# Kernel tuning notes

Hardware: AMD Instinct MI355X
Metric: run time of the kernel (lower is better)

The kernel has to match this reference:

```python
import jax, jax.numpy as jnp
import numpy as np
from jax import lax

B, N, C = 32, 512, 512   # N must be 8*8*8 (Convpass reshape)
H, DH = 8, 64            # heads, head_dim
ADIM = 8                 # adapter dim
MLP = 4096
EPS = 1e-5
SCALE = DH ** -0.5


def _ln(x, g, b):
    m = jnp.mean(x, axis=-1, keepdims=True)
    v = jnp.mean((x - m) ** 2, axis=-1, keepdims=True)
    return (x - m) * lax.rsqrt(v + EPS) * g + b


def _qgelu(x):
    return x * jax.nn.sigmoid(1.702 * x)


def _convpass(x, dw, db, cw, cb, uw, ub):
    # x: [B,N,C] -> down [B,N,ADIM]
    d = _qgelu(jnp.einsum('bnc,ca->bna', x, dw) + db)
    p = d.reshape(B, 8, 8, 8, ADIM).transpose(0, 4, 1, 2, 3)  # NCDHW
    p = lax.conv_general_dilated(
        p, cw, window_strides=(1, 1, 1), padding='SAME',
        dimension_numbers=('NCDHW', 'OIDHW', 'NCDHW')) + cb[None, :, None, None, None]
    p = p.transpose(0, 2, 3, 4, 1).reshape(B, N, ADIM)
    return jnp.einsum('bna,ac->bnc', _qgelu(p), uw) + ub


def _attn(x, qkv_w, proj_w, proj_b):
    qkv = jnp.einsum('bnc,ck->bnk', x, qkv_w)            # [B,N,3C]
    qkv = qkv.reshape(B, N, 3, H, DH)
    q, k, v = (qkv[:, :, i].transpose(0, 2, 1, 3) for i in range(3))  # [B,H,N,DH]
    a = jax.nn.softmax(jnp.einsum('bhnd,bhmd->bhnm', q, k) * SCALE, axis=-1)
    o = jnp.einsum('bhnm,bhmd->bhnd', a, v).transpose(0, 2, 1, 3).reshape(B, N, C)
    return jnp.einsum('bnc,ck->bnk', o, proj_w) + proj_b


def setup_inputs() -> dict:
    key = jax.random.key(0)
    ks = jax.random.split(key, 24)
    r = lambda i, shape, s=0.02: jax.random.normal(ks[i], shape, jnp.float32) * s
    inp = {
        'x': jax.random.normal(ks[0], (B, N, C), jnp.float32),
        'pos': jax.random.normal(ks[1], (B, N, C), jnp.float32),
        'ln1_g': jnp.ones((C,), jnp.float32), 'ln1_b': jnp.zeros((C,), jnp.float32),
        'qkv_w': r(2, (C, 3 * C)),
        'proj_w': r(3, (C, C)), 'proj_b': jnp.zeros((C,), jnp.float32),
        'cp1_down_w': r(4, (C, ADIM)), 'cp1_down_b': jnp.zeros((ADIM,), jnp.float32),
        'cp1_conv_w': r(5, (ADIM, ADIM, 3, 3, 3), 0.1), 'cp1_conv_b': jnp.zeros((ADIM,), jnp.float32),
        'cp1_up_w': r(6, (ADIM, C)), 'cp1_up_b': jnp.zeros((C,), jnp.float32),
        'ln2_g': jnp.ones((C,), jnp.float32), 'ln2_b': jnp.zeros((C,), jnp.float32),
        'ff_w1': r(7, (C, MLP)), 'ff_b1': jnp.zeros((MLP,), jnp.float32),
        'ff_w2': r(8, (MLP, C)), 'ff_b2': jnp.zeros((C,), jnp.float32),
        'cp2_down_w': r(9, (C, ADIM)), 'cp2_down_b': jnp.zeros((ADIM,), jnp.float32),
        'cp2_conv_w': r(10, (ADIM, ADIM, 3, 3, 3), 0.1), 'cp2_conv_b': jnp.zeros((ADIM,), jnp.float32),
        'cp2_up_w': r(11, (ADIM, C)), 'cp2_up_b': jnp.zeros((C,), jnp.float32),
    }
    return inp


def reference(x, pos, ln1_g, ln1_b, qkv_w, proj_w, proj_b,
              cp1_down_w, cp1_down_b, cp1_conv_w, cp1_conv_b, cp1_up_w, cp1_up_b,
              ln2_g, ln2_b, ff_w1, ff_b1, ff_w2, ff_b2,
              cp2_down_w, cp2_down_b, cp2_conv_w, cp2_conv_b, cp2_up_w, cp2_up_b):
    x = x + pos
    # attention stage: Residual(PreNormDrop(LN, SelfAttn, Convpass)), dropout=identity (eval)
    h = _ln(x, ln1_g, ln1_b)
    x = x + _attn(h, qkv_w, proj_w, proj_b) + _convpass(h, cp1_down_w, cp1_down_b, cp1_conv_w, cp1_conv_b, cp1_up_w, cp1_up_b)
    # FFN stage: Residual(PreNorm(LN, FFN, Convpass))
    h = _ln(x, ln2_g, ln2_b)
    ffn = jnp.einsum('bnm,mc->bnc', jax.nn.gelu(jnp.einsum('bnc,cm->bnm', h, ff_w1) + ff_b1, approximate=False), ff_w2) + ff_b2
    x = x + ffn + _convpass(h, cp2_down_w, cp2_down_b, cp2_conv_w, cp2_conv_b, cp2_up_w, cp2_up_b)
    return x
```

## Files before the change

kernel.cpp:

```cpp
#include <hip/hip_runtime.h>
#include <math.h>

typedef __bf16 bf16_t;
typedef __bf16 bf16x8 __attribute__((ext_vector_type(8)));
typedef float f32x4 __attribute__((ext_vector_type(4)));

constexpr int kB   = 32;
constexpr int kN   = 512;
constexpr int kC   = 512;
constexpr int kH   = 8;
constexpr int kAD  = 8;
constexpr int kMLP = 4096;
constexpr int kBN  = kB * kN;
constexpr float kEPS   = 1e-5f;
constexpr float kSCALE = 0.125f;

__device__ __forceinline__ float qgelu_f(float x) {
    return x / (1.f + __expf(-1.702f * x));
}
__device__ __forceinline__ float gelu_f(float x) {
    float u = 1.5957691216f * x * (1.f + 0.044715f * x * x);
    float e = __expf(u);
    float th = 1.f - 2.f / (e + 1.f);
    return 0.5f * x * (1.f + th);
}

__device__ __forceinline__ void gld_lds16(const void* g, void* l) {
    typedef const __attribute__((address_space(1))) unsigned int* gp_t;
    typedef __attribute__((address_space(3))) unsigned int* lp_t;
    __builtin_amdgcn_global_load_lds((gp_t)(unsigned long long)g,
                                     (lp_t)(unsigned)(unsigned long long)l,
                                     16, 0, 0);
}

__global__ __launch_bounds__(256) void k_addln(
    const float* __restrict__ x, const float* __restrict__ pos,
    const float* __restrict__ g, const float* __restrict__ be,
    float* __restrict__ xout, bf16_t* __restrict__ hout,
    const float* __restrict__ cpv, const float* __restrict__ uwp,
    const float* __restrict__ ubp)
{
    int row = blockIdx.x, tid = threadIdx.x;
    size_t base = (size_t)row * kC;
    __shared__ float s8[8];
    if (cpv) {
        if (tid < 8) s8[tid] = cpv[(size_t)row * 8 + tid];
        __syncthreads();
    }
    float v0 = x[base + tid], v1 = x[base + tid + 256];
    if (pos) { v0 += pos[base + tid]; v1 += pos[base + tid + 256]; }
    if (cpv) {
        float u0 = ubp[tid], u1 = ubp[tid + 256];
        #pragma unroll
        for (int a = 0; a < 8; a++) {
            u0 += s8[a] * uwp[a * kC + tid];
            u1 += s8[a] * uwp[a * kC + tid + 256];
        }
        v0 += u0; v1 += u1;
    }
    if (xout) { xout[base + tid] = v0; xout[base + tid + 256] = v1; }
    float s = v0 + v1, q = v0 * v0 + v1 * v1;
    #pragma unroll
    for (int o = 32; o > 0; o >>= 1) {
        s += __shfl_down(s, o);
        q += __shfl_down(q, o);
    }
    __shared__ float ss[4], sq[4], mrs[2];
    int wv = tid >> 6, ln = tid & 63;
    if (!ln) { ss[wv] = s; sq[wv] = q; }
    __syncthreads();
    if (!tid) {
        float ts = ss[0] + ss[1] + ss[2] + ss[3];
        float tq = sq[0] + sq[1] + sq[2] + sq[3];
        float m = ts * (1.f / kC);
        float var = tq * (1.f / kC) - m * m;
        mrs[0] = m; mrs[1] = rsqrtf(var + kEPS);
    }
    __syncthreads();
    float m = mrs[0], r = mrs[1];
    hout[base + tid]       = (bf16_t)((v0 - m) * r * g[tid] + be[tid]);
    hout[base + tid + 256] = (bf16_t)((v1 - m) * r * g[tid + 256] + be[tid + 256]);
}

__global__ __launch_bounds__(256) void k_transpose_all(
    const float* __restrict__ qkvw, const float* __restrict__ projw,
    const float* __restrict__ fw1,  const float* __restrict__ fw2,
    bf16_t* __restrict__ qkvT, bf16_t* __restrict__ projT,
    bf16_t* __restrict__ fw1T, bf16_t* __restrict__ fw2T)
{
    int id = blockIdx.x;
    const float* w; bf16_t* wt; int K, N, bx, by;
    if (id < 768)       { w = qkvw; wt = qkvT; K = 512;  N = 1536; bx = id % 48;  by = id / 48; }
    else if (id < 1024) { id -= 768;  w = projw; wt = projT; K = 512;  N = 512;  bx = id % 16;  by = id / 16; }
    else if (id < 3072) { id -= 1024; w = fw1;   wt = fw1T;  K = 512;  N = 4096; bx = id % 128; by = id / 128; }
    else                { id -= 3072; w = fw2;   wt = fw2T;  K = 4096; N = 512;  bx = id % 16;  by = id / 16; }
    __shared__ float t[32][33];
    int n0 = bx * 32, k0 = by * 32;
    int tx = threadIdx.x & 31, ty = threadIdx.x >> 5;
    #pragma unroll
    for (int j = 0; j < 32; j += 8)
        t[ty + j][tx] = w[(size_t)(k0 + ty + j) * N + n0 + tx];
    __syncthreads();
    #pragma unroll
    for (int j = 0; j < 32; j += 8)
        wt[(size_t)(n0 + ty + j) * K + k0 + tx] = (bf16_t)t[tx][ty + j];
}

template <int ACT, bool HASB, bool HASR, int OMODE, int K, int LDA, int LDB, int NC>
__global__ __launch_bounds__(256) void k_gemm(
    const bf16_t* __restrict__ A, const bf16_t* __restrict__ Bt,
    const float* __restrict__ bias, const float* __restrict__ res,
    void* __restrict__ outv)
{
    __shared__ bf16_t As[2][128 * 32];
    __shared__ bf16_t Bs[2][128 * 32];
    int tid = threadIdx.x;
    int col0 = blockIdx.x * 128, row0 = blockIdx.y * 128;
    int w = tid >> 6, l = tid & 63;
    int rw0 = (w & 1) * 64, cw0 = (w >> 1) * 64;
    int lr = tid >> 2;
    int lc = (((tid & 3) ^ ((tid >> 3) & 3)) * 8);

    f32x4 acc[4][4];
    #pragma unroll
    for (int i = 0; i < 4; i++)
        #pragma unroll
        for (int j = 0; j < 4; j++)
            acc[i][j] = (f32x4){0.f, 0.f, 0.f, 0.f};

    const bf16_t* Ag  = A  + (size_t)(row0 + lr) * LDA + lc;
    const bf16_t* Ag2 = A  + (size_t)(row0 + 64 + lr) * LDA + lc;
    const bf16_t* Bg  = Bt + (size_t)(col0 + lr) * LDB + lc;
    const bf16_t* Bg2 = Bt + (size_t)(col0 + 64 + lr) * LDB + lc;

    int am = rw0 + (l & 15);
    int bn = cw0 + (l & 15);
    int kq = (l >> 4) * 8;
    int kqA = kq ^ (((am >> 1) & 3) << 3);
    int kqB = kq ^ (((bn >> 1) & 3) << 3);

    for (int k0 = 0; k0 < K; k0 += 64) {
        gld_lds16(Ag + k0, &As[0][tid * 8]);
        gld_lds16(Ag2 + k0, &As[0][2048 + tid * 8]);
        gld_lds16(Bg + k0, &Bs[0][tid * 8]);
        gld_lds16(Bg2 + k0, &Bs[0][2048 + tid * 8]);
        gld_lds16(Ag + k0 + 32, &As[1][tid * 8]);
        gld_lds16(Ag2 + k0 + 32, &As[1][2048 + tid * 8]);
        gld_lds16(Bg + k0 + 32, &Bs[1][tid * 8]);
        gld_lds16(Bg2 + k0 + 32, &Bs[1][2048 + tid * 8]);
        __syncthreads();
        #pragma unroll
        for (int ks = 0; ks < 2; ks++) {
            bf16x8 af[4], bfr[4];
            #pragma unroll
            for (int mt = 0; mt < 4; mt++)
                af[mt] = *(const bf16x8*)&As[ks][(am + mt * 16) * 32 + kqA];
            #pragma unroll
            for (int nt = 0; nt < 4; nt++)
                bfr[nt] = *(const bf16x8*)&Bs[ks][(bn + nt * 16) * 32 + kqB];
            #pragma unroll
            for (int mt = 0; mt < 4; mt++)
                #pragma unroll
                for (int nt = 0; nt < 4; nt++)
                    acc[mt][nt] = __builtin_amdgcn_mfma_f32_16x16x32_bf16(
                        af[mt], bfr[nt], acc[mt][nt], 0, 0, 0);
        }
        __syncthreads();
    }

    #pragma unroll
    for (int mt = 0; mt < 4; mt++) {
        int rowb = row0 + rw0 + mt * 16 + (l >> 4) * 4;
        #pragma unroll
        for (int nt = 0; nt < 4; nt++) {
            int col = col0 + cw0 + nt * 16 + (l & 15);
            float bv = HASB ? bias[col] : 0.f;
            #pragma unroll
            for (int p = 0; p < 4; p++) {
                float v = acc[mt][nt][p] + bv;
                if (ACT == 1) v = qgelu_f(v);
                if (ACT == 2) v = gelu_f(v);
                int r = rowb + p;
                if (OMODE == 0) {
                    if (HASR) v += res[(size_t)r * NC + col];
                    ((float*)outv)[(size_t)r * NC + col] = v;
                } else if (OMODE == 1) {
                    ((bf16_t*)outv)[(size_t)r * NC + col] = (bf16_t)v;
                } else {
                    int bb = r >> 9, n = r & 511;
                    int which = col >> 9, hd = (col >> 6) & 7, d = col & 63;
                    ((bf16_t*)outv)[(((size_t)(bb * 8 + hd) * 3 + which) << 15)
                                    + n * 64 + d] = (bf16_t)v;
                }
            }
        }
    }
}

__global__ __launch_bounds__(256) void k_attn(
    const bf16_t* __restrict__ qkvb, bf16_t* __restrict__ obuf)
{
    __shared__ bf16_t Ks[64 * 72];
    __shared__ bf16_t Vt[64 * 72];
    __shared__ bf16_t Ps[4][32 * 72];
    int bid = blockIdx.x;
    int qb = bid & 3, h = (bid >> 2) & 7, b = bid >> 5;
    int t = threadIdx.x, w = t >> 6, l = t & 63;
    const bf16_t* qp = qkvb + (((size_t)(b * 8 + h) * 3) << 15);
    const bf16_t* kp = qp + (1 << 15);
    const bf16_t* vp = qp + (2 << 15);
    int q0 = qb * 128 + w * 32;
    int l15 = l & 15, lq = (l >> 4) * 8;

    bf16x8 aq[2][2];
    #pragma unroll
    for (int mt = 0; mt < 2; mt++)
        #pragma unroll
        for (int kh = 0; kh < 2; kh++)
            aq[mt][kh] = *(const bf16x8*)(qp + (size_t)(q0 + mt * 16 + l15) * 64
                                          + kh * 32 + lq);

    f32x4 o[2][4];
    float m_run[2][4], l_run[2][4];
    #pragma unroll
    for (int mt = 0; mt < 2; mt++) {
        #pragma unroll
        for (int dt = 0; dt < 4; dt++) o[mt][dt] = (f32x4){0.f, 0.f, 0.f, 0.f};
        #pragma unroll
        for (int p = 0; p < 4; p++) { m_run[mt][p] = -1e30f; l_run[mt][p] = 0.f; }
    }

    int sr = t >> 2, scc = (t & 3) * 16;
    for (int kt = 0; kt < 8; kt++) {
        if (kt) __syncthreads();
        {
            const bf16_t* ks = kp + (size_t)(kt * 64 + sr) * 64 + scc;
            *(uint4*)&Ks[sr * 72 + scc]     = *(const uint4*)ks;
            *(uint4*)&Ks[sr * 72 + scc + 8] = *(const uint4*)(ks + 8);
            const bf16_t* vs = vp + (size_t)(kt * 64 + sr) * 64 + scc;
            bf16x8 v0 = *(const bf16x8*)vs;
            bf16x8 v1 = *(const bf16x8*)(vs + 8);
            #pragma unroll
            for (int e = 0; e < 8; e++) {
                Vt[(scc + e) * 72 + sr]     = v0[e];
                Vt[(scc + 8 + e) * 72 + sr] = v1[e];
            }
        }
        __syncthreads();
        #pragma unroll
        for (int mt = 0; mt < 2; mt++) {
            f32x4 sc[4];
            #pragma unroll
            for (int nt = 0; nt < 4; nt++) sc[nt] = (f32x4){0.f, 0.f, 0.f, 0.f};
            #pragma unroll
            for (int nt = 0; nt < 4; nt++)
                #pragma unroll
                for (int kh = 0; kh < 2; kh++) {
                    bf16x8 bk = *(const bf16x8*)&Ks[(nt * 16 + l15) * 72
                                                    + kh * 32 + lq];
                    sc[nt] = __builtin_amdgcn_mfma_f32_16x16x32_bf16(
                        aq[mt][kh], bk, sc[nt], 0, 0, 0);
                }
            #pragma unroll
            for (int nt = 0; nt < 4; nt++)
                #pragma unroll
                for (int p = 0; p < 4; p++) sc[nt][p] *= kSCALE;

            float mx[4], alpha[4], rs[4];
            #pragma unroll
            for (int p = 0; p < 4; p++) {
                float m4 = fmaxf(fmaxf(sc[0][p], sc[1][p]),
                                 fmaxf(sc[2][p], sc[3][p]));
                #pragma unroll
                for (int off = 1; off < 16; off <<= 1)
                    m4 = fmaxf(m4, __shfl_xor(m4, off));
                float mn = fmaxf(m_run[mt][p], m4);
                alpha[p] = __expf(m_run[mt][p] - mn);
                m_run[mt][p] = mn;
                mx[p] = mn;
                rs[p] = 0.f;
            }
            int prow = mt * 16 + (l >> 4) * 4;
            #pragma unroll
            for (int nt = 0; nt < 4; nt++)
                #pragma unroll
                for (int p = 0; p < 4; p++) {
                    float pv = __expf(sc[nt][p] - mx[p]);
                    rs[p] += pv;
                    Ps[w][(prow + p) * 72 + nt * 16 + l15] = (bf16_t)pv;
                }
            #pragma unroll
            for (int p = 0; p < 4; p++) {
                float r = rs[p];
                #pragma unroll
                for (int off = 1; off < 16; off <<= 1)
                    r += __shfl_xor(r, off);
                l_run[mt][p] = l_run[mt][p] * alpha[p] + r;
                #pragma unroll
                for (int dt = 0; dt < 4; dt++) o[mt][dt][p] *= alpha[p];
            }
            bf16x8 ap[2];
            #pragma unroll
            for (int kh = 0; kh < 2; kh++)
                ap[kh] = *(const bf16x8*)&Ps[w][(mt * 16 + l15) * 72
                                                + kh * 32 + lq];
            #pragma unroll
            for (int dt = 0; dt < 4; dt++)
                #pragma unroll
                for (int kh = 0; kh < 2; kh++) {
                    bf16x8 bv = *(const bf16x8*)&Vt[(dt * 16 + l15) * 72
                                                    + kh * 32 + lq];
                    o[mt][dt] = __builtin_amdgcn_mfma_f32_16x16x32_bf16(
                        ap[kh], bv, o[mt][dt], 0, 0, 0);
                }
        }
    }
    #pragma unroll
    for (int mt = 0; mt < 2; mt++)
        #pragma unroll
        for (int dt = 0; dt < 4; dt++)
            #pragma unroll
            for (int p = 0; p < 4; p++) {
                int q = q0 + mt * 16 + (l >> 4) * 4 + p;
                int col = h * 64 + dt * 16 + l15;
                float v = o[mt][dt][p] / l_run[mt][p];
                obuf[((size_t)b * 512 + q) * 512 + col] = (bf16_t)v;
            }
}

__global__ __launch_bounds__(256) void k_down(
    const bf16_t* __restrict__ h, const float* __restrict__ dw,
    const float* __restrict__ db, float* __restrict__ outp)
{
    __shared__ float sdw[kC * kAD];
    int t = threadIdx.x;
    for (int i = t; i < kC * kAD; i += 256) sdw[i] = dw[i];
    __syncthreads();
    int gt = blockIdx.x * 256 + t;
    int row = gt >> 3, a = gt & 7;
    const bf16x8* hr = (const bf16x8*)(h + (size_t)row * kC);
    float acc = 0.f;
    for (int k8 = 0; k8 < kC / 8; k8++) {
        bf16x8 hv = hr[k8];
        #pragma unroll
        for (int e = 0; e < 8; e++)
            acc += (float)hv[e] * sdw[(k8 * 8 + e) * kAD + a];
    }
    outp[gt] = qgelu_f(acc + db[a]);
}

__global__ __launch_bounds__(512) void k_conv(
    const float* __restrict__ inp, const float* __restrict__ cw,
    const float* __restrict__ cb, float* __restrict__ outp)
{
    __shared__ float si[512 * 9];
    __shared__ float sw[8 * 8 * 27];
    int b = blockIdx.x, t = threadIdx.x;
    for (int i = t; i < 512 * 8; i += 512) {
        int n = i >> 3, a = i & 7;
        si[n * 9 + a] = inp[(size_t)b * 4096 + i];
    }
    for (int i = t; i < 1728; i += 512) sw[i] = cw[i];
    __syncthreads();
    int z = t >> 6, y = (t >> 3) & 7, xx = t & 7;
    float acc[8];
    #pragma unroll
    for (int ao = 0; ao < 8; ao++) acc[ao] = cb[ao];
    for (int dz = -1; dz <= 1; dz++) {
        int zz = z + dz; if ((unsigned)zz > 7u) continue;
        for (int dy = -1; dy <= 1; dy++) {
            int yy = y + dy; if ((unsigned)yy > 7u) continue;
            for (int dx = -1; dx <= 1; dx++) {
                int xn = xx + dx; if ((unsigned)xn > 7u) continue;
                int nn = zz * 64 + yy * 8 + xn;
                int wo = ((dz + 1) * 3 + (dy + 1)) * 3 + (dx + 1);
                #pragma unroll
                for (int ai = 0; ai < 8; ai++) {
                    float iv = si[nn * 9 + ai];
                    #pragma unroll
                    for (int ao = 0; ao < 8; ao++)
                        acc[ao] += iv * sw[(ao * 8 + ai) * 27 + wo];
                }
            }
        }
    }
    #pragma unroll
    for (int ao = 0; ao < 8; ao++)
        outp[(size_t)b * 4096 + t * 8 + ao] = qgelu_f(acc[ao]);
}

__global__ __launch_bounds__(256) void k_up(
    const float* __restrict__ pa, const float* __restrict__ uw,
    const float* __restrict__ ub, float* __restrict__ xbuf)
{
    __shared__ float s[8];
    int row = blockIdx.x, t = threadIdx.x;
    if (t < 8) s[t] = pa[(size_t)row * kAD + t];
    __syncthreads();
    #pragma unroll
    for (int rep = 0; rep < 2; rep++) {
        int c = t + rep * 256;
        float acc = ub[c];
        #pragma unroll
        for (int a = 0; a < 8; a++) acc += s[a] * uw[a * kC + c];
        xbuf[(size_t)row * kC + c] += acc;
    }
}

extern "C" void kernel_launch(void* const* d_in, const int* in_sizes, int n_in,
                              void* d_out, int out_size, void* d_ws, size_t ws_size,
                              hipStream_t stream)
{
    const float* x     = (const float*)d_in[0];
    const float* pos   = (const float*)d_in[1];
    const float* ln1g  = (const float*)d_in[2];
    const float* ln1b  = (const float*)d_in[3];
    const float* qkvw  = (const float*)d_in[4];
    const float* projw = (const float*)d_in[5];
    const float* projb = (const float*)d_in[6];
    const float* dw1   = (const float*)d_in[7];
    const float* db1   = (const float*)d_in[8];
    const float* cw1   = (const float*)d_in[9];
    const float* cb1   = (const float*)d_in[10];
    const float* uw1   = (const float*)d_in[11];
    const float* ub1   = (const float*)d_in[12];
    const float* ln2g  = (const float*)d_in[13];
    const float* ln2b  = (const float*)d_in[14];
    const float* fw1   = (const float*)d_in[15];
    const float* fb1   = (const float*)d_in[16];
    const float* fw2   = (const float*)d_in[17];
    const float* fb2   = (const float*)d_in[18];
    const float* dw2   = (const float*)d_in[19];
    const float* db2   = (const float*)d_in[20];
    const float* cw2   = (const float*)d_in[21];
    const float* cb2   = (const float*)d_in[22];
    const float* uw2   = (const float*)d_in[23];
    const float* ub2   = (const float*)d_in[24];
    float* out = (float*)d_out;

    char* wsb = (char*)d_ws;
    float*  xbuf = (float*)wsb;
    bf16_t* hb   = (bf16_t*)(wsb + 33554432);
    bf16_t* obuf = (bf16_t*)(wsb + 50331648);
    bf16_t* qkvb = (bf16_t*)(wsb + 67108864);
    bf16_t* midb = (bf16_t*)(wsb + 50331648);
    bf16_t* qkvT = (bf16_t*)(wsb + 117440512);
    bf16_t* projT= (bf16_t*)(wsb + 119013376);
    bf16_t* fw1T = (bf16_t*)(wsb + 119537664);
    bf16_t* fw2T = (bf16_t*)(wsb + 123731968);
    float*  cpa  = (float*)(wsb + 127926272);
    float*  cpb  = (float*)(wsb + 128450560);

    k_transpose_all<<<5120, 256, 0, stream>>>(
        qkvw, projw, fw1, fw2, qkvT, projT, fw1T, fw2T);

    k_addln<<<kBN, 256, 0, stream>>>(x, pos, ln1g, ln1b, xbuf, hb,
                                     nullptr, nullptr, nullptr);

    k_gemm<0, false, false, 2, 512, 512, 512, 1536>
        <<<dim3(12, 128), 256, 0, stream>>>(hb, qkvT, nullptr, nullptr, qkvb);
    k_attn<<<kB * kH * 4, 256, 0, stream>>>(qkvb, obuf);
    k_gemm<0, true, true, 0, 512, 512, 512, 512>
        <<<dim3(4, 128), 256, 0, stream>>>(obuf, projT, projb, xbuf, xbuf);

    k_down<<<kBN * kAD / 256, 256, 0, stream>>>(hb, dw1, db1, cpa);
    k_conv<<<kB, 512, 0, stream>>>(cpa, cw1, cb1, cpb);

    k_addln<<<kBN, 256, 0, stream>>>(xbuf, nullptr, ln2g, ln2b, xbuf, hb,
                                     cpb, uw1, ub1);

    k_down<<<kBN * kAD / 256, 256, 0, stream>>>(hb, dw2, db2, cpa);
    k_conv<<<kB, 512, 0, stream>>>(cpa, cw2, cb2, cpb);
    k_up<<<kBN, 256, 0, stream>>>(cpb, uw2, ub2, xbuf);

    k_gemm<2, true, false, 1, 512, 512, 512, 2048>
        <<<dim3(16, 128), 256, 0, stream>>>(hb, fw1T, fb1, nullptr, midb);
    k_gemm<0, false, true, 0, 2048, 2048, 4096, 512>
        <<<dim3(4, 128), 256, 0, stream>>>(midb, fw2T, nullptr, xbuf, xbuf);
    k_gemm<2, true, false, 1, 512, 512, 512, 2048>
        <<<dim3(16, 128), 256, 0, stream>>>(hb, fw1T + (size_t)2048 * 512,
                                            fb1 + 2048, nullptr, midb);
    k_gemm<0, true, true, 0, 2048, 2048, 4096, 512>
        <<<dim3(4, 128), 256, 0, stream>>>(midb, fw2T + 2048, fb2, xbuf, out);
}
```

Measured before the change: 639.9 us.

## Store V transposed from QKV GEMM and compute transposed attention from registers

The QKV GEMM epilogue now writes V transposed (d-major) using packed 4-wide stores. The attention kernel then loads K and V^T fragments straight from global memory into registers, so the shared-memory staging, the scalar transpose and the block barriers are gone. It also computes S^T so each lane owns one query column, which cuts the softmax reductions to two shuffles, and it pre-scales Q by the softmax scale. The P tile goes through a small per-warp LDS buffer, and the output is written with packed stores. The cost is that K and V are re-read from global or L2 by every warp instead of being shared through LDS, and rounding Q after scaling changes precision slightly.

```diff
diff --git a/kernel.cpp b/kernel.cpp
--- a/kernel.cpp
+++ b/kernel.cpp
@@ -3,6 +3,7 @@
 
 typedef __bf16 bf16_t;
 typedef __bf16 bf16x8 __attribute__((ext_vector_type(8)));
+typedef __bf16 bf16x4 __attribute__((ext_vector_type(4)));
 typedef float f32x4 __attribute__((ext_vector_type(4)));
 
 constexpr int kB   = 32;
@@ -23,6 +24,12 @@
     float e = __expf(u);
     float th = 1.f - 2.f / (e + 1.f);
     return 0.5f * x * (1.f + th);
+}
+
+__device__ __forceinline__ unsigned pk2(float a, float b) {
+    union { bf16_t h[2]; unsigned u; } z;
+    z.h[0] = (bf16_t)a; z.h[1] = (bf16_t)b;
+    return z.u;
 }
 
 __device__ __forceinline__ void gld_lds16(const void* g, void* l) {
@@ -175,22 +182,34 @@
         for (int nt = 0; nt < 4; nt++) {
             int col = col0 + cw0 + nt * 16 + (l & 15);
             float bv = HASB ? bias[col] : 0.f;
-            #pragma unroll
-            for (int p = 0; p < 4; p++) {
-                float v = acc[mt][nt][p] + bv;
-                if (ACT == 1) v = qgelu_f(v);
-                if (ACT == 2) v = gelu_f(v);
-                int r = rowb + p;
-                if (OMODE == 0) {
-                    if (HASR) v += res[(size_t)r * NC + col];
-                    ((float*)outv)[(size_t)r * NC + col] = v;
-                } else if (OMODE == 1) {
-                    ((bf16_t*)outv)[(size_t)r * NC + col] = (bf16_t)v;
+            if (OMODE == 2) {
+                int which = col >> 9, hd = (col >> 6) & 7, d = col & 63;
+                size_t hb = ((size_t)((rowb >> 9) * 8 + hd) * 3 + which) << 15;
+                int n0 = rowb & 511;
+                if (which == 2) {
+                    bf16x4 pk;
+                    #pragma unroll
+                    for (int p = 0; p < 4; p++) pk[p] = (bf16_t)acc[mt][nt][p];
+                    *(bf16x4*)((bf16_t*)outv + hb + (size_t)d * 512 + n0) = pk;
                 } else {
-                    int bb = r >> 9, n = r & 511;
-                    int which = col >> 9, hd = (col >> 6) & 7, d = col & 63;
-                    ((bf16_t*)outv)[(((size_t)(bb * 8 + hd) * 3 + which) << 15)
-                                    + n * 64 + d] = (bf16_t)v;
+                    #pragma unroll
+                    for (int p = 0; p < 4; p++)
+                        ((bf16_t*)outv)[hb + (size_t)(n0 + p) * 64 + d] =
+                            (bf16_t)acc[mt][nt][p];
+                }
+            } else {
+                #pragma unroll
+                for (int p = 0; p < 4; p++) {
+                    float v = acc[mt][nt][p] + bv;
+                    if (ACT == 1) v = qgelu_f(v);
+                    if (ACT == 2) v = gelu_f(v);
+                    int r = rowb + p;
+                    if (OMODE == 0) {
+                        if (HASR) v += res[(size_t)r * NC + col];
+                        ((float*)outv)[(size_t)r * NC + col] = v;
+                    } else {
+                        ((bf16_t*)outv)[(size_t)r * NC + col] = (bf16_t)v;
+                    }
                 }
             }
         }
@@ -200,53 +219,53 @@
 __global__ __launch_bounds__(256) void k_attn(
     const bf16_t* __restrict__ qkvb, bf16_t* __restrict__ obuf)
 {
-    __shared__ bf16_t Ks[64 * 72];
-    __shared__ bf16_t Vt[64 * 72];
-    __shared__ bf16_t Ps[4][32 * 72];
+    __shared__ __align__(16) unsigned Ps[4][16 * 36];
     int bid = blockIdx.x;
     int qb = bid & 3, h = (bid >> 2) & 7, b = bid >> 5;
     int t = threadIdx.x, w = t >> 6, l = t & 63;
-    const bf16_t* qp = qkvb + (((size_t)(b * 8 + h) * 3) << 15);
-    const bf16_t* kp = qp + (1 << 15);
-    const bf16_t* vp = qp + (2 << 15);
+    const bf16_t* qp  = qkvb + (((size_t)(b * 8 + h) * 3) << 15);
+    const bf16_t* kp  = qp + (1 << 15);
+    const bf16_t* vtp = qp + (2 << 15);
     int q0 = qb * 128 + w * 32;
-    int l15 = l & 15, lq = (l >> 4) * 8;
+    int l15 = l & 15, g = l >> 4, lq = g * 8;
+    unsigned* psw = &Ps[w][0];
 
     bf16x8 aq[2][2];
     #pragma unroll
     for (int mt = 0; mt < 2; mt++)
         #pragma unroll
-        for (int kh = 0; kh < 2; kh++)
-            aq[mt][kh] = *(const bf16x8*)(qp + (size_t)(q0 + mt * 16 + l15) * 64
-                                          + kh * 32 + lq);
+        for (int kh = 0; kh < 2; kh++) {
+            bf16x8 qv = *(const bf16x8*)(qp + (size_t)(q0 + mt * 16 + l15) * 64
+                                         + kh * 32 + lq);
+            #pragma unroll
+            for (int e = 0; e < 8; e++) qv[e] = (bf16_t)((float)qv[e] * kSCALE);
+            aq[mt][kh] = qv;
+        }
 
     f32x4 o[2][4];
-    float m_run[2][4], l_run[2][4];
+    float m_run[2], l_run[2];
     #pragma unroll
     for (int mt = 0; mt < 2; mt++) {
+        m_run[mt] = -1e30f; l_run[mt] = 0.f;
         #pragma unroll
         for (int dt = 0; dt < 4; dt++) o[mt][dt] = (f32x4){0.f, 0.f, 0.f, 0.f};
-        #pragma unroll
-        for (int p = 0; p < 4; p++) { m_run[mt][p] = -1e30f; l_run[mt][p] = 0.f; }
-    }
-
-    int sr = t >> 2, scc = (t & 3) * 16;
+    }
+
     for (int kt = 0; kt < 8; kt++) {
-        if (kt) __syncthreads();
-        {
-            const bf16_t* ks = kp + (size_t)(kt * 64 + sr) * 64 + scc;
-            *(uint4*)&Ks[sr * 72 + scc]     = *(const uint4*)ks;
-            *(uint4*)&Ks[sr * 72 + scc + 8] = *(const uint4*)(ks + 8);
-            const bf16_t* vs = vp + (size_t)(kt * 64 + sr) * 64 + scc;
-            bf16x8 v0 = *(const bf16x8*)vs;
-            bf16x8 v1 = *(const bf16x8*)(vs + 8);
-            #pragma unroll
-            for (int e = 0; e < 8; e++) {
-                Vt[(scc + e) * 72 + sr]     = v0[e];
-                Vt[(scc + 8 + e) * 72 + sr] = v1[e];
-            }
-        }
-        __syncthreads();
+        bf16x8 kf[4][2], vf[4][2];
+        #pragma unroll
+        for (int nt = 0; nt < 4; nt++)
+            #pragma unroll
+            for (int kh = 0; kh < 2; kh++)
+                kf[nt][kh] = *(const bf16x8*)(kp
+                    + (size_t)(kt * 64 + nt * 16 + l15) * 64 + kh * 32 + lq);
+        #pragma unroll
+        for (int dt = 0; dt < 4; dt++)
+            #pragma unroll
+            for (int kh = 0; kh < 2; kh++)
+                vf[dt][kh] = *(const bf16x8*)(vtp
+                    + (size_t)(dt * 16 + l15) * 512 + kt * 64 + kh * 32 + lq);
+
         #pragma unroll
         for (int mt = 0; mt < 2; mt++) {
             f32x4 sc[4];
@@ -255,77 +274,66 @@
             #pragma unroll
             for (int nt = 0; nt < 4; nt++)
                 #pragma unroll
-                for (int kh = 0; kh < 2; kh++) {
-                    bf16x8 bk = *(const bf16x8*)&Ks[(nt * 16 + l15) * 72
-                                                    + kh * 32 + lq];
+                for (int kh = 0; kh < 2; kh++)
                     sc[nt] = __builtin_amdgcn_mfma_f32_16x16x32_bf16(
-                        aq[mt][kh], bk, sc[nt], 0, 0, 0);
+                        kf[nt][kh], aq[mt][kh], sc[nt], 0, 0, 0);
+            float mx = sc[0][0];
+            #pragma unroll
+            for (int nt = 0; nt < 4; nt++)
+                #pragma unroll
+                for (int p = 0; p < 4; p++) mx = fmaxf(mx, sc[nt][p]);
+            mx = fmaxf(mx, __shfl_xor(mx, 16));
+            mx = fmaxf(mx, __shfl_xor(mx, 32));
+            float mn = fmaxf(m_run[mt], mx);
+            float alpha = __expf(m_run[mt] - mn);
+            m_run[mt] = mn;
+            float rs = 0.f;
+            #pragma unroll
+            for (int nt = 0; nt < 4; nt++)
+                #pragma unroll
+                for (int p = 0; p < 4; p++) {
+                    float pv = __expf(sc[nt][p] - mn);
+                    sc[nt][p] = pv; rs += pv;
                 }
-            #pragma unroll
-            for (int nt = 0; nt < 4; nt++)
-                #pragma unroll
-                for (int p = 0; p < 4; p++) sc[nt][p] *= kSCALE;
-
-            float mx[4], alpha[4], rs[4];
-            #pragma unroll
-            for (int p = 0; p < 4; p++) {
-                float m4 = fmaxf(fmaxf(sc[0][p], sc[1][p]),
-                                 fmaxf(sc[2][p], sc[3][p]));
-                #pragma unroll
-                for (int off = 1; off < 16; off <<= 1)
-                    m4 = fmaxf(m4, __shfl_xor(m4, off));
-                float mn = fmaxf(m_run[mt][p], m4);
-                alpha[p] = __expf(m_run[mt][p] - mn);
-                m_run[mt][p] = mn;
-                mx[p] = mn;
-                rs[p] = 0.f;
+            rs += __shfl_xor(rs, 16);
+            rs += __shfl_xor(rs, 32);
+            l_run[mt] = l_run[mt] * alpha + rs;
+            #pragma unroll
+            for (int dt = 0; dt < 4; dt++)
+                #pragma unroll
+                for (int p = 0; p < 4; p++) o[mt][dt][p] *= alpha;
+            #pragma unroll
+            for (int nt = 0; nt < 4; nt++) {
+                uint2 dw;
+                dw.x = pk2(sc[nt][0], sc[nt][1]);
+                dw.y = pk2(sc[nt][2], sc[nt][3]);
+                *(uint2*)&psw[l15 * 36 + nt * 8 + g * 2] = dw;
             }
-            int prow = mt * 16 + (l >> 4) * 4;
-            #pragma unroll
-            for (int nt = 0; nt < 4; nt++)
-                #pragma unroll
-                for (int p = 0; p < 4; p++) {
-                    float pv = __expf(sc[nt][p] - mx[p]);
-                    rs[p] += pv;
-                    Ps[w][(prow + p) * 72 + nt * 16 + l15] = (bf16_t)pv;
-                }
-            #pragma unroll
-            for (int p = 0; p < 4; p++) {
-                float r = rs[p];
-                #pragma unroll
-                for (int off = 1; off < 16; off <<= 1)
-                    r += __shfl_xor(r, off);
-                l_run[mt][p] = l_run[mt][p] * alpha[p] + r;
-                #pragma unroll
-                for (int dt = 0; dt < 4; dt++) o[mt][dt][p] *= alpha[p];
+            asm volatile("" ::: "memory");
+            bf16x8 pf0 = *(const bf16x8*)&psw[l15 * 36 + g * 4];
+            bf16x8 pf1 = *(const bf16x8*)&psw[l15 * 36 + 16 + g * 4];
+            #pragma unroll
+            for (int dt = 0; dt < 4; dt++) {
+                o[mt][dt] = __builtin_amdgcn_mfma_f32_16x16x32_bf16(
+                    vf[dt][0], pf0, o[mt][dt], 0, 0, 0);
+                o[mt][dt] = __builtin_amdgcn_mfma_f32_16x16x32_bf16(
+                    vf[dt][1], pf1, o[mt][dt], 0, 0, 0);
             }
-            bf16x8 ap[2];
-            #pragma unroll
-            for (int kh = 0; kh < 2; kh++)
-                ap[kh] = *(const bf16x8*)&Ps[w][(mt * 16 + l15) * 72
-                                                + kh * 32 + lq];
-            #pragma unroll
-            for (int dt = 0; dt < 4; dt++)
-                #pragma unroll
-                for (int kh = 0; kh < 2; kh++) {
-                    bf16x8 bv = *(const bf16x8*)&Vt[(dt * 16 + l15) * 72
-                                                    + kh * 32 + lq];
-                    o[mt][dt] = __builtin_amdgcn_mfma_f32_16x16x32_bf16(
-                        ap[kh], bv, o[mt][dt], 0, 0, 0);
-                }
-        }
-    }
-    #pragma unroll
-    for (int mt = 0; mt < 2; mt++)
-        #pragma unroll
-        for (int dt = 0; dt < 4; dt++)
-            #pragma unroll
-            for (int p = 0; p < 4; p++) {
-                int q = q0 + mt * 16 + (l >> 4) * 4 + p;
-                int col = h * 64 + dt * 16 + l15;
-                float v = o[mt][dt][p] / l_run[mt][p];
-                obuf[((size_t)b * 512 + q) * 512 + col] = (bf16_t)v;
-            }
+            asm volatile("" ::: "memory");
+        }
+    }
+    #pragma unroll
+    for (int mt = 0; mt < 2; mt++) {
+        float inv = 1.f / l_run[mt];
+        size_t rbase = ((size_t)b * 512 + q0 + mt * 16 + l15) * 512 + h * 64;
+        #pragma unroll
+        for (int dt = 0; dt < 4; dt++) {
+            bf16x4 pk;
+            #pragma unroll
+            for (int p = 0; p < 4; p++) pk[p] = (bf16_t)(o[mt][dt][p] * inv);
+            *(bf16x4*)&obuf[rbase + dt * 16 + g * 4] = pk;
+        }
+    }
 }
 
 __global__ __launch_bounds__(256) void k_down(
```

Result: no change. 637.7 us (-0.3%).
